# Optimization experiments

Measured on AMD Instinct MI355X. Metric: run time of the kernel, lower is better.

## Reference

```python
import jax, jax.numpy as jnp
import numpy as np

# DeepSeek-V2 MLA dims (one tensor-parallel shard of 8)
H = 5120          # hidden size
S = 2048          # seq len
B = 1
NH = 16           # 128 heads / 8 devices
Q_LORA = 1536
KV_LORA = 512
NOPE = 128
ROPE = 64
QK = NOPE + ROPE  # 192 per-head q/k dim
VD = 128          # v head dim
DEVICE_NUM = 8
EPS = 1e-6


def rms_norm(x, w):
    v = jnp.mean(jnp.square(x.astype(jnp.float32)), axis=-1, keepdims=True)
    return (x * jax.lax.rsqrt(v + EPS)).astype(x.dtype) * w


def rope_cos_sin(position_ids, dim=ROPE, base=10000.0):
    inv_freq = 1.0 / (base ** (jnp.arange(0, dim, 2, dtype=jnp.float32) / dim))
    freqs = position_ids.astype(jnp.float32)[..., None] * inv_freq       # [B,S,dim/2]
    emb = jnp.concatenate([freqs, freqs], axis=-1)                        # [B,S,dim]
    return jnp.cos(emb), jnp.sin(emb)


def apply_rope(x, cos, sin):
    # DeepSeek interleaved reorder: view(b,h,s,d//2,2).transpose(-1,-2).reshape
    b, h, s, d = x.shape
    x = x.reshape(b, h, s, d // 2, 2).transpose(0, 1, 2, 4, 3).reshape(b, h, s, d)
    x1, x2 = x[..., : d // 2], x[..., d // 2:]
    rot = jnp.concatenate([-x2, x1], axis=-1)
    return x * cos[:, None] + rot * sin[:, None]


def setup_inputs() -> dict:
    key = jax.random.key(0)
    ks = jax.random.split(key, 8)
    sc = 0.02
    hidden_states = jax.random.normal(ks[0], (B, S, H), dtype=jnp.float32)
    position_ids = jnp.arange(S, dtype=jnp.int64 if jax.config.jax_enable_x64 else jnp.int32)[None, :].repeat(B, 0)
    attention_mask = jnp.triu(jnp.full((S, S), -1e9, dtype=jnp.float32), 1)[None, None]
    return {
        "hidden_states": hidden_states,
        "position_ids": position_ids,
        "attention_mask": attention_mask,
        "ln_w": jnp.ones((H,), jnp.float32),
        "q_a_w": jax.random.normal(ks[1], (Q_LORA, H), jnp.float32) * sc,
        "q_a_ln_w": jnp.ones((Q_LORA,), jnp.float32),
        "q_b_w": jax.random.normal(ks[2], (NH * QK, Q_LORA), jnp.float32) * sc,
        "kv_a_w": jax.random.normal(ks[3], (KV_LORA + ROPE, H), jnp.float32) * sc,
        "kv_a_ln_w": jnp.ones((KV_LORA,), jnp.float32),
        "kv_b_w": jax.random.normal(ks[4], (NH * (NOPE + VD), KV_LORA), jnp.float32) * sc,
        "o_w": jax.random.normal(ks[5], (H, NH * VD), jnp.float32) * sc,
    }


def reference(hidden_states, position_ids, attention_mask, ln_w, q_a_w, q_a_ln_w,
              q_b_w, kv_a_w, kv_a_ln_w, kv_b_w, o_w):
    b, s, _ = hidden_states.shape
    residual = hidden_states * (1.0 / DEVICE_NUM)
    x = rms_norm(hidden_states, ln_w)

    # Q path: low-rank down-proj + RMSNorm + up-proj
    q = rms_norm(x @ q_a_w.T, q_a_ln_w) @ q_b_w.T                # [b,s,NH*QK]
    q = q.reshape(b, s, NH, QK).transpose(0, 2, 1, 3)            # [b,NH,s,QK]
    q_nope, q_pe = q[..., :NOPE], q[..., NOPE:]

    # KV path: compressed latent + shared rope key
    ckv = x @ kv_a_w.T                                           # [b,s,KV_LORA+ROPE]
    c_kv, k_pe = ckv[..., :KV_LORA], ckv[..., KV_LORA:]
    k_pe = k_pe.reshape(b, s, 1, ROPE).transpose(0, 2, 1, 3)     # [b,1,s,ROPE]
    kv = rms_norm(c_kv, kv_a_ln_w) @ kv_b_w.T                    # [b,s,NH*(NOPE+VD)]
    kv = kv.reshape(b, s, NH, NOPE + VD).transpose(0, 2, 1, 3)
    k_nope, v = kv[..., :NOPE], kv[..., NOPE:]

    cos, sin = rope_cos_sin(position_ids)
    q_pe = apply_rope(q_pe, cos, sin)
    k_pe = apply_rope(k_pe, cos, sin)

    k = jnp.concatenate([k_nope, jnp.broadcast_to(k_pe, (b, NH, s, ROPE))], axis=-1)
    qf = jnp.concatenate([q_nope, q_pe], axis=-1)

    scores = jnp.einsum('bhqd,bhkd->bhqk', qf, k) * (1.0 / np.sqrt(QK))
    scores = scores + attention_mask
    probs = jax.nn.softmax(scores, axis=-1)
    attn = jnp.einsum('bhqk,bhkd->bhqd', probs, v)               # [b,NH,s,VD]

    out = attn.transpose(0, 2, 1, 3).reshape(b, s, NH * VD) @ o_w.T
    hidden = residual + out
    return hidden.astype(jnp.float32), k.astype(jnp.float32), v.astype(jnp.float32)
```

## Files before the change

kernel.cpp:

```cpp
#include <hip/hip_runtime.h>
#include <math.h>

typedef unsigned short u16;
typedef unsigned int u32;
typedef __attribute__((ext_vector_type(8))) short short8;
typedef __attribute__((ext_vector_type(4))) float f32x4;

#define NHEADS 16
static const int S      = 2048;
static const int Hd     = 5120;
static const int QLORA  = 1536;
static const int KVLORA = 512;
static const int NQK    = 192;
static const int NVD    = 128;
static const int QDIM   = 3072;
static const int KVDIM  = 4096;
static const int NFUSE  = 2176;

__device__ __forceinline__ u16 f2bf(float f) {
    union { float f; u32 u; } v; v.f = f;
    u32 r = v.u + 0x7FFFu + ((v.u >> 16) & 1u);
    return (u16)(r >> 16);
}
__device__ __forceinline__ float bf2f(u16 h) {
    union { u32 u; float f; } v; v.u = (u32)h << 16; return v.f;
}

__global__ void convert_all_kernel(const float* __restrict__ o_w,
                                   const float* __restrict__ q_a_w,
                                   const float* __restrict__ kv_a_w,
                                   const float* __restrict__ q_b_w,
                                   const float* __restrict__ kv_b_w,
                                   u16* __restrict__ o_wb, u16* __restrict__ Wf,
                                   u16* __restrict__ q_b_wb, u16* __restrict__ kv_b_wb) {
    long c = (long)blockIdx.x * 256 + threadIdx.x;
    const float* src; u16* dst; long nsrcc;
    if (c < 2621440L)      { src = o_w;    dst = o_wb;            nsrcc = 2621440L; }
    else if (c < 4587520L) { c -= 2621440L; src = q_a_w; dst = Wf; nsrcc = 1966080L; }
    else if (c < 5406720L) { c -= 4587520L; src = kv_a_w; dst = Wf + 7864320L; nsrcc = 737280L; }
    else if (c < 6586368L) { c -= 5406720L; src = q_b_w;  dst = q_b_wb;  nsrcc = 1179648L; }
    else if (c < 7110656L) { c -= 6586368L; src = kv_b_w; dst = kv_b_wb; nsrcc = 524288L; }
    else return;
    union { u16 h[4]; uint2 u; } p;
    if (c < nsrcc) {
        float4 v = *(const float4*)(src + c * 4);
        p.h[0] = f2bf(v.x); p.h[1] = f2bf(v.y); p.h[2] = f2bf(v.z); p.h[3] = f2bf(v.w);
    } else {
        p.h[0] = p.h[1] = p.h[2] = p.h[3] = 0;
    }
    *(uint2*)(dst + c * 4) = p.u;
}

__global__ void rmsnorm_bf16_kernel(const float* in, const float* __restrict__ w,
                                    u16* out, int D, int in_stride, int out_stride) {
    int row = blockIdx.x;
    const float* x = in + (size_t)row * in_stride;
    u16* y = out + (size_t)row * out_stride;
    float ss = 0.f;
    for (int i = threadIdx.x; i < D; i += blockDim.x) { float v = x[i]; ss += v * v; }
    #pragma unroll
    for (int off = 32; off > 0; off >>= 1) ss += __shfl_xor(ss, off);
    __shared__ float wsum[8];
    int wid = threadIdx.x >> 6, lane = threadIdx.x & 63;
    if (lane == 0) wsum[wid] = ss;
    __syncthreads();
    float tot = 0.f;
    int nw = blockDim.x >> 6;
    for (int i = 0; i < nw; ++i) tot += wsum[i];
    float scale = rsqrtf(tot / (float)D + 1e-6f);
    for (int i = threadIdx.x; i < D; i += blockDim.x) y[i] = f2bf(x[i] * scale * w[i]);
}

__global__ void rms_qkv_kernel(const u16* __restrict__ CF,
                               const float* __restrict__ qw, const float* __restrict__ kw,
                               u16* __restrict__ QAn, u16* __restrict__ CKVN) {
    const int row = blockIdx.x;
    const u16* x; u16* y; const float* w; int D;
    if (blockIdx.y == 0) {
        x = CF + (size_t)row * NFUSE;          y = QAn + (size_t)row * QLORA;
        w = qw; D = QLORA;
    } else {
        x = CF + (size_t)row * NFUSE + QLORA;  y = CKVN + (size_t)row * KVLORA;
        w = kw; D = KVLORA;
    }
    float ss = 0.f;
    for (int i = threadIdx.x; i < D; i += blockDim.x) { float v = bf2f(x[i]); ss += v * v; }
    #pragma unroll
    for (int off = 32; off > 0; off >>= 1) ss += __shfl_xor(ss, off);
    __shared__ float wsum[4];
    int wid = threadIdx.x >> 6, lane = threadIdx.x & 63;
    if (lane == 0) wsum[wid] = ss;
    __syncthreads();
    float tot = wsum[0] + wsum[1] + wsum[2] + wsum[3];
    float scale = rsqrtf(tot / (float)D + 1e-6f);
    for (int i = threadIdx.x; i < D; i += blockDim.x) y[i] = f2bf(bf2f(x[i]) * scale * w[i]);
}

template<int BM, bool SWZ, bool OBF>
__global__ __launch_bounds__(256) void gemm64_k(
    const u16* __restrict__ A, const u16* __restrict__ B, void* __restrict__ Cv,
    int M, int N, int K, const float* __restrict__ resid) {
    constexpr int MR = BM / 32;
    constexpr int ALOADS = (BM * 128) / 4096;
    __shared__ u16 As[2][BM * 64];
    __shared__ u16 Bs[2][128 * 64];

    int bm, bn;
    if constexpr (SWZ) {
        const int lin = blockIdx.x + blockIdx.y * gridDim.x;
        const int nwg = gridDim.x * gridDim.y;
        const int xcd = lin & 7, off = lin >> 3;
        const int q = nwg >> 3, r = nwg & 7;
        const int wg = (xcd < r ? xcd * (q + 1) : r * (q + 1) + (xcd - r) * q) + off;
        bm = (wg % gridDim.y) * BM;
        bn = (wg / gridDim.y) * 128;
    } else {
        bm = blockIdx.y * BM;
        bn = blockIdx.x * 128;
    }

    const int tid = threadIdx.x;
    const int w = tid >> 6, lane = tid & 63;
    const int wr = w >> 1, wc = w & 1;
    const int fr = lane & 15, kg = lane >> 4;
    const int swz = (fr & 7) << 4;

    f32x4 acc[MR][4];
    #pragma unroll
    for (int i = 0; i < MR; ++i)
        #pragma unroll
        for (int j = 0; j < 4; ++j) acc[i][j] = (f32x4){0.f, 0.f, 0.f, 0.f};

    const size_t K2 = (size_t)K * 2;

    auto STAGE = [&](int buf, int kt) {
        const char* ga = (const char*)A + ((size_t)bm * K + (size_t)kt * 64) * 2;
        const char* gb = (const char*)B + ((size_t)bn * K + (size_t)kt * 64) * 2;
        #pragma unroll
        for (int j = 0; j < ALOADS; ++j) {
            const int D = j * 4096 + tid * 16;
            const int r = D >> 7, c = (D & 127) ^ ((r & 7) << 4);
            __builtin_amdgcn_global_load_lds(
                (const __attribute__((address_space(1))) void*)(ga + (size_t)r * K2 + c),
                (__attribute__((address_space(3))) void*)((char*)&As[buf][0] + D), 16, 0, 0);
        }
        #pragma unroll
        for (int j = 0; j < 4; ++j) {
            const int D = j * 4096 + tid * 16;
            const int r = D >> 7, c = (D & 127) ^ ((r & 7) << 4);
            __builtin_amdgcn_global_load_lds(
                (const __attribute__((address_space(1))) void*)(gb + (size_t)r * K2 + c),
                (__attribute__((address_space(3))) void*)((char*)&Bs[buf][0] + D), 16, 0, 0);
        }
    };
    auto COMP = [&](int buf) {
        #pragma unroll
        for (int s = 0; s < 2; ++s) {
            short8 af[MR], bfr[4];
            #pragma unroll
            for (int i = 0; i < MR; ++i) {
                const int row = wr * (BM / 2) + i * 16 + fr;
                af[i] = *(const short8*)((const char*)&As[buf][0] +
                         row * 128 + ((s * 64 + kg * 16) ^ swz));
            }
            #pragma unroll
            for (int i = 0; i < 4; ++i) {
                const int row = wc * 64 + i * 16 + fr;
                bfr[i] = *(const short8*)((const char*)&Bs[buf][0] +
                          row * 128 + ((s * 64 + kg * 16) ^ swz));
            }
            #pragma unroll
            for (int mi = 0; mi < MR; ++mi)
                #pragma unroll
                for (int ni = 0; ni < 4; ++ni)
                    acc[mi][ni] = __builtin_amdgcn_mfma_f32_16x16x32_bf16(
                        af[mi], bfr[ni], acc[mi][ni], 0, 0, 0);
        }
    };

    const int nk = K >> 6;
    STAGE(0, 0);
    asm volatile("s_waitcnt vmcnt(0)" ::: "memory");
    __builtin_amdgcn_s_barrier();
    for (int kt = 0; kt < nk; ++kt) {
        if (kt + 1 < nk) STAGE((kt + 1) & 1, kt + 1);
        COMP(kt & 1);
        asm volatile("s_waitcnt vmcnt(0)" ::: "memory");
        __builtin_amdgcn_s_barrier();
    }

    #pragma unroll
    for (int mi = 0; mi < MR; ++mi)
        #pragma unroll
        for (int ni = 0; ni < 4; ++ni)
            #pragma unroll
            for (int r2 = 0; r2 < 4; ++r2) {
                int row = bm + wr * (BM / 2) + mi * 16 + kg * 4 + r2;
                int col = bn + wc * 64 + ni * 16 + fr;
                size_t idx = (size_t)row * N + col;
                float v = acc[mi][ni][r2];
                if constexpr (OBF) {
                    ((u16*)Cv)[idx] = f2bf(v);
                } else {
                    if (resid) v += resid[idx] * 0.125f;
                    ((float*)Cv)[idx] = v;
                }
            }
}

__global__ __launch_bounds__(256) void gemm_qkv64_kernel(
    const u16* __restrict__ QAn, const u16* __restrict__ CKVN,
    const u16* __restrict__ q_b_wb, const u16* __restrict__ kv_b_wb,
    u16* __restrict__ Qbf, u16* __restrict__ KVb) {
    __shared__ u16 As[2][64 * 64];
    __shared__ u16 Bs[2][128 * 64];
    const bool isQ = blockIdx.x < 24;
    const u16* A = isQ ? QAn : CKVN;
    const u16* B = isQ ? q_b_wb : kv_b_wb;
    const int K = isQ ? QLORA : KVLORA;
    const int bn = (isQ ? blockIdx.x : blockIdx.x - 24) * 128;
    const int bm = blockIdx.y * 64;

    const int tid = threadIdx.x;
    const int w = tid >> 6, lane = tid & 63;
    const int wr = w >> 1, wc = w & 1;
    const int fr = lane & 15, kg = lane >> 4;
    const int swz = (fr & 7) << 4;

    f32x4 acc[2][4];
    #pragma unroll
    for (int i = 0; i < 2; ++i)
        #pragma unroll
        for (int j = 0; j < 4; ++j) acc[i][j] = (f32x4){0.f, 0.f, 0.f, 0.f};

    const size_t K2 = (size_t)K * 2;

    auto STAGE = [&](int buf, int kt) {
        const char* ga = (const char*)A + ((size_t)bm * K + (size_t)kt * 64) * 2;
        const char* gb = (const char*)B + ((size_t)bn * K + (size_t)kt * 64) * 2;
        #pragma unroll
        for (int j = 0; j < 2; ++j) {
            const int D = j * 4096 + tid * 16;
            const int r = D >> 7, c = (D & 127) ^ ((r & 7) << 4);
            __builtin_amdgcn_global_load_lds(
                (const __attribute__((address_space(1))) void*)(ga + (size_t)r * K2 + c),
                (__attribute__((address_space(3))) void*)((char*)&As[buf][0] + D), 16, 0, 0);
        }
        #pragma unroll
        for (int j = 0; j < 4; ++j) {
            const int D = j * 4096 + tid * 16;
            const int r = D >> 7, c = (D & 127) ^ ((r & 7) << 4);
            __builtin_amdgcn_global_load_lds(
                (const __attribute__((address_space(1))) void*)(gb + (size_t)r * K2 + c),
                (__attribute__((address_space(3))) void*)((char*)&Bs[buf][0] + D), 16, 0, 0);
        }
    };
    auto COMP = [&](int buf) {
        #pragma unroll
        for (int s = 0; s < 2; ++s) {
            short8 af[2], bfr[4];
            #pragma unroll
            for (int i = 0; i < 2; ++i) {
                const int row = wr * 32 + i * 16 + fr;
                af[i] = *(const short8*)((const char*)&As[buf][0] +
                         row * 128 + ((s * 64 + kg * 16) ^ swz));
            }
            #pragma unroll
            for (int i = 0; i < 4; ++i) {
                const int row = wc * 64 + i * 16 + fr;
                bfr[i] = *(const short8*)((const char*)&Bs[buf][0] +
                          row * 128 + ((s * 64 + kg * 16) ^ swz));
            }
            #pragma unroll
            for (int mi = 0; mi < 2; ++mi)
                #pragma unroll
                for (int ni = 0; ni < 4; ++ni)
                    acc[mi][ni] = __builtin_amdgcn_mfma_f32_16x16x32_bf16(
                        af[mi], bfr[ni], acc[mi][ni], 0, 0, 0);
        }
    };

    const int nk = K >> 6;
    STAGE(0, 0);
    asm volatile("s_waitcnt vmcnt(0)" ::: "memory");
    __builtin_amdgcn_s_barrier();
    for (int kt = 0; kt < nk; ++kt) {
        if (kt + 1 < nk) STAGE((kt + 1) & 1, kt + 1);
        COMP(kt & 1);
        asm volatile("s_waitcnt vmcnt(0)" ::: "memory");
        __builtin_amdgcn_s_barrier();
    }

    #pragma unroll
    for (int mi = 0; mi < 2; ++mi)
        #pragma unroll
        for (int ni = 0; ni < 4; ++ni)
            #pragma unroll
            for (int r2 = 0; r2 < 4; ++r2) {
                int row = bm + wr * 32 + mi * 16 + kg * 4 + r2;
                int col = bn + wc * 64 + ni * 16 + fr;
                float v = acc[mi][ni][r2];
                if (isQ) {
                    size_t idx = ((size_t)(col / 192) * S + row) * 192 + (col % 192);
                    Qbf[idx] = f2bf(v);
                } else {
                    KVb[(size_t)row * KVDIM + col] = f2bf(v);
                }
            }
}

__global__ void rope_q_inplace_kernel(u16* __restrict__ Qbf, const int* __restrict__ pos) {
    const int s = blockIdx.x;
    const int t = threadIdx.x;
    const int hh = t >> 5, j = t & 31;
    float ps = (float)pos[s];
    float inv_freq = 1.0f / powf(10000.0f, (float)j * (1.0f / 32.0f));
    float ang = ps * inv_freq;
    float c = cosf(ang), sn = sinf(ang);
    u16* base = Qbf + ((size_t)hh * S + s) * NQK;
    float a = bf2f(base[128 + 2 * j]), b = bf2f(base[128 + 2 * j + 1]);
    __syncthreads();
    base[128 + j] = f2bf(a * c - b * sn);
    base[160 + j] = f2bf(b * c + a * sn);
}

__global__ __launch_bounds__(256) void build_kv64_kernel(
    const u16* __restrict__ KVb, const u16* __restrict__ CF,
    const int* __restrict__ pos_ids,
    float* __restrict__ Kout, float* __restrict__ Vout,
    u16* __restrict__ Kbf, u16* __restrict__ Vtb) {
    const int s0 = blockIdx.x * 64;
    const int h  = blockIdx.y;
    const int t  = threadIdx.x;
    __shared__ u16 T[64][132];

    #pragma unroll
    for (int it = 0; it < 4; ++it) {
        int i = t + it * 256;
        int row = i >> 4, c8 = (i & 15) * 8;
        int s = s0 + row;
        union { uint4 u; u16 hx[8]; } v;
        v.u = *(const uint4*)(KVb + (size_t)s * KVDIM + h * 256 + c8);
        size_t kidx = ((size_t)h * S + s) * NQK + c8;
        *(uint4*)(Kbf + kidx) = v.u;
        float4 f0 = {bf2f(v.hx[0]), bf2f(v.hx[1]), bf2f(v.hx[2]), bf2f(v.hx[3])};
        float4 f1 = {bf2f(v.hx[4]), bf2f(v.hx[5]), bf2f(v.hx[6]), bf2f(v.hx[7])};
        *(float4*)(Kout + kidx) = f0;
        *(float4*)(Kout + kidx + 4) = f1;
    }
    #pragma unroll
    for (int it = 0; it < 4; ++it) {
        int i = t + it * 256;
        int row = i >> 4, c8 = (i & 15) * 8;
        int s = s0 + row;
        union { uint4 u; uint2 d[2]; u16 hx[8]; } v;
        v.u = *(const uint4*)(KVb + (size_t)s * KVDIM + h * 256 + 128 + c8);
        *(uint2*)&T[row][c8]     = v.d[0];
        *(uint2*)&T[row][c8 + 4] = v.d[1];
        size_t vidx = ((size_t)h * S + s) * NVD + c8;
        float4 f0 = {bf2f(v.hx[0]), bf2f(v.hx[1]), bf2f(v.hx[2]), bf2f(v.hx[3])};
        float4 f1 = {bf2f(v.hx[4]), bf2f(v.hx[5]), bf2f(v.hx[6]), bf2f(v.hx[7])};
        *(float4*)(Vout + vidx) = f0;
        *(float4*)(Vout + vidx + 4) = f1;
    }
    #pragma unroll
    for (int it = 0; it < 8; ++it) {
        int i = t + it * 256;
        int row = i >> 5, j = i & 31;
        int s = s0 + row;
        float ps = (float)pos_ids[s];
        float inv_freq = 1.0f / powf(10000.0f, (float)j * (1.0f / 32.0f));
        float ang = ps * inv_freq;
        float c = cosf(ang), sn = sinf(ang);
        u32 pr = *(const u32*)(CF + (size_t)s * NFUSE + QLORA + KVLORA + 2 * j);
        float a = bf2f((u16)pr), b = bf2f((u16)(pr >> 16));
        float k0 = a * c - b * sn;
        float k1 = b * c + a * sn;
        size_t kidx = ((size_t)h * S + s) * NQK;
        Kout[kidx + 128 + j] = k0;
        Kout[kidx + 160 + j] = k1;
        Kbf[kidx + 128 + j] = f2bf(k0);
        Kbf[kidx + 160 + j] = f2bf(k1);
    }
    __syncthreads();
    const int d = t >> 1, half = t & 1;
    #pragma unroll
    for (int c = 0; c < 4; ++c) {
        u16 tmp[8];
        #pragma unroll
        for (int e = 0; e < 8; ++e) tmp[e] = T[half * 32 + c * 8 + e][d];
        *(uint4*)(Vtb + ((size_t)h * NVD + d) * S + s0 + half * 32 + c * 8) = *(uint4*)tmp;
    }
}

__global__ __launch_bounds__(256) void attn_mfma_kernel(
    const u16* __restrict__ Qbf, const u16* __restrict__ Kb,
    const u16* __restrict__ Vtb, u16* __restrict__ ATb) {
    const int h = blockIdx.y;
    const int q0 = (gridDim.x - 1 - blockIdx.x) * 64;
    const int tid = threadIdx.x;
    const int w = tid >> 6, lane = tid & 63;
    const int fr = lane & 15, kg = lane >> 4;

    __shared__ __align__(16) u16 Ks[2][64 * 192];
    __shared__ __align__(16) u16 Vts[2][128 * 64];

    int kSrc[6], vSrc[4];
    #pragma unroll
    for (int i = 0; i < 6; ++i) {
        int D = (w * 6 + i) * 1024 + lane * 16;
        int row = D / 384, wb = D - row * 384;
        kSrc[i] = row * 384 + (wb ^ ((row & 7) << 4));
    }
    #pragma unroll
    for (int i = 0; i < 4; ++i) {
        int D = (w * 4 + i) * 1024 + lane * 16;
        int row = D >> 7, wb = D & 127;
        vSrc[i] = row * (S * 2) + (wb ^ ((row & 7) << 4));
    }
    const char* Kg = (const char*)(Kb + (size_t)h * S * NQK);
    const char* Vg = (const char*)(Vtb + (size_t)h * NVD * S);

    auto STAGE = [&](int buf, int kt) {
        const size_t krow = (size_t)kt * 64;
        #pragma unroll
        for (int i = 0; i < 6; ++i)
            __builtin_amdgcn_global_load_lds(
                (const __attribute__((address_space(1))) void*)(Kg + krow * 384 + kSrc[i]),
                (__attribute__((address_space(3))) void*)((char*)&Ks[buf][0] + (w * 6 + i) * 1024), 16, 0, 0);
        #pragma unroll
        for (int i = 0; i < 4; ++i)
            __builtin_amdgcn_global_load_lds(
                (const __attribute__((address_space(1))) void*)(Vg + krow * 2 + vSrc[i]),
                (__attribute__((address_space(3))) void*)((char*)&Vts[buf][0] + (w * 4 + i) * 1024), 16, 0, 0);
    };

    short8 qf[6];
    {
        const u16* qrow = Qbf + ((size_t)h * S + q0 + w * 16 + fr) * NQK;
        #pragma unroll
        for (int kb = 0; kb < 6; ++kb)
            qf[kb] = *(const short8*)(qrow + kb * 32 + kg * 8);
    }

    f32x4 o[8];
    #pragma unroll
    for (int ni = 0; ni < 8; ++ni) o[ni] = (f32x4){0.f, 0.f, 0.f, 0.f};
    float mrow = -1e30f, lrow = 0.f;
    const float scale = 0.0721687836487032f;
    const int qg = q0 + w * 16 + fr;
    const int swz = (fr & 7) << 4;
    const int nt = (q0 >> 6) + 1;

    STAGE(0, 0);
    asm volatile("s_waitcnt vmcnt(0)" ::: "memory");
    __builtin_amdgcn_s_barrier();

    for (int t = 0; t < nt; ++t) {
        if (t + 1 < nt) STAGE((t + 1) & 1, t + 1);
        const int buf = t & 1;
        const int k0 = t * 64;

        f32x4 sacc[4];
        #pragma unroll
        for (int mi = 0; mi < 4; ++mi) sacc[mi] = (f32x4){0.f, 0.f, 0.f, 0.f};
        __builtin_amdgcn_s_setprio(1);
        #pragma unroll
        for (int mi = 0; mi < 4; ++mi)
            #pragma unroll
            for (int kb = 0; kb < 6; ++kb) {
                const short8 kf = *(const short8*)((const char*)&Ks[buf][0] +
                    (mi * 16 + fr) * 384 + ((kb * 64 + kg * 16) ^ swz));
                sacc[mi] = __builtin_amdgcn_mfma_f32_16x16x32_bf16(kf, qf[kb], sacc[mi], 0, 0, 0);
            }
        __builtin_amdgcn_s_setprio(0);

        const bool diag = (k0 == q0);
        float p[4][4];
        float mx = -1e30f;
        #pragma unroll
        for (int mi = 0; mi < 4; ++mi)
            #pragma unroll
            for (int r = 0; r < 4; ++r) {
                float v = sacc[mi][r] * scale;
                if (diag && (k0 + mi * 16 + kg * 4 + r > qg)) v = -1e30f;
                p[mi][r] = v;
                mx = fmaxf(mx, v);
            }
        mx = fmaxf(mx, __shfl_xor(mx, 16));
        mx = fmaxf(mx, __shfl_xor(mx, 32));
        const bool noresc = __all(mx <= mrow + 8.0f);
        float mnew = noresc ? mrow : fmaxf(mrow, mx);
        float psum = 0.f;
        #pragma unroll
        for (int mi = 0; mi < 4; ++mi)
            #pragma unroll
            for (int r = 0; r < 4; ++r) {
                float e = __expf(p[mi][r] - mnew);
                p[mi][r] = e;
                psum += e;
            }
        psum += __shfl_xor(psum, 16);
        psum += __shfl_xor(psum, 32);
        if (noresc) {
            lrow += psum;
        } else {
            float corr = __expf(mrow - mnew);
            lrow = lrow * corr + psum;
            mrow = mnew;
            float corr_r[4];
            #pragma unroll
            for (int r = 0; r < 4; ++r) corr_r[r] = __shfl(corr, kg * 4 + r);
            #pragma unroll
            for (int ni = 0; ni < 8; ++ni) {
                o[ni][0] *= corr_r[0]; o[ni][1] *= corr_r[1];
                o[ni][2] *= corr_r[2]; o[ni][3] *= corr_r[3];
            }
        }

        u32 pk0[4], pk1[4];
        #pragma unroll
        for (int mi = 0; mi < 4; ++mi) {
            pk0[mi] = (u32)f2bf(p[mi][0]) | ((u32)f2bf(p[mi][1]) << 16);
            pk1[mi] = (u32)f2bf(p[mi][2]) | ((u32)f2bf(p[mi][3]) << 16);
        }
        const int srcA = 2 * (kg & 1) * 16 + fr;
        const int srcB = srcA + 16;
        const int hsel = kg >> 1;
        short8 pa[2];
        #pragma unroll
        for (int ks = 0; ks < 2; ++ks) {
            u32 a0 = (u32)__shfl((int)pk0[ks * 2], srcA), b0 = (u32)__shfl((int)pk0[ks * 2 + 1], srcA);
            u32 a1 = (u32)__shfl((int)pk1[ks * 2], srcA), b1 = (u32)__shfl((int)pk1[ks * 2 + 1], srcA);
            u32 a2 = (u32)__shfl((int)pk0[ks * 2], srcB), b2 = (u32)__shfl((int)pk0[ks * 2 + 1], srcB);
            u32 a3 = (u32)__shfl((int)pk1[ks * 2], srcB), b3 = (u32)__shfl((int)pk1[ks * 2 + 1], srcB);
            union { u32 u[4]; short8 s8; } cvt;
            cvt.u[0] = hsel ? b0 : a0;
            cvt.u[1] = hsel ? b1 : a1;
            cvt.u[2] = hsel ? b2 : a2;
            cvt.u[3] = hsel ? b3 : a3;
            pa[ks] = cvt.s8;
        }

        __builtin_amdgcn_s_setprio(1);
        #pragma unroll
        for (int ks = 0; ks < 2; ++ks)
            #pragma unroll
            for (int ni = 0; ni < 8; ++ni) {
                const short8 vf = *(const short8*)((const char*)&Vts[buf][0] +
                    (ni * 16 + fr) * 128 + ((ks * 64 + kg * 16) ^ swz));
                o[ni] = __builtin_amdgcn_mfma_f32_16x16x32_bf16(pa[ks], vf, o[ni], 0, 0, 0);
            }
        __builtin_amdgcn_s_setprio(0);

        asm volatile("s_waitcnt vmcnt(0)" ::: "memory");
        __builtin_amdgcn_s_barrier();
    }

    float inv = 1.f / lrow;
    float inv_r[4];
    #pragma unroll
    for (int r = 0; r < 4; ++r) inv_r[r] = __shfl(inv, kg * 4 + r);
    u16* outp = ATb + (size_t)(q0 + w * 16 + kg * 4) * (NHEADS * NVD) + h * NVD + fr;
    #pragma unroll
    for (int ni = 0; ni < 8; ++ni)
        #pragma unroll
        for (int r = 0; r < 4; ++r)
            outp[(size_t)r * (NHEADS * NVD) + ni * 16] = f2bf(o[ni][r] * inv_r[r]);
}

extern "C" void kernel_launch(void* const* d_in, const int* in_sizes, int n_in,
                              void* d_out, int out_size, void* d_ws, size_t ws_size,
                              hipStream_t stream) {
    (void)in_sizes; (void)n_in; (void)out_size; (void)ws_size;
    const float* hidden    = (const float*)d_in[0];
    const int*   pos       = (const int*)d_in[1];
    const float* ln_w      = (const float*)d_in[3];
    const float* q_a_w     = (const float*)d_in[4];
    const float* q_a_ln_w  = (const float*)d_in[5];
    const float* q_b_w     = (const float*)d_in[6];
    const float* kv_a_w    = (const float*)d_in[7];
    const float* kv_a_ln_w = (const float*)d_in[8];
    const float* kv_b_w    = (const float*)d_in[9];
    const float* o_w       = (const float*)d_in[10];

    float* OUT_H = (float*)d_out;
    float* OUT_K = OUT_H + (size_t)S * Hd;
    float* OUT_V = OUT_K + (size_t)NHEADS * S * NQK;

    char* ws = (char*)d_ws;
    u16*   o_wb    = (u16*)(ws);
    u16*   Wf      = (u16*)(ws + 20971520);
    u16*   Qbf     = (u16*)(ws + 20971520);
    u16*   Vtb     = (u16*)(ws + 33554432);
    u16*   Xb      = (u16*)(ws + 43253760);
    u16*   Kbf     = (u16*)(ws + 43253760);
    u16*   ATb     = (u16*)(ws + 55836672);
    u16*   CF      = (u16*)(ws + 64225280);
    u16*   QAn     = (u16*)(ws + 73138176);
    u16*   CKVN    = (u16*)(ws + 79429632);
    u16*   q_b_wb  = (u16*)(ws + 81526784);
    u16*   kv_b_wb = (u16*)(ws + 90963968);
    u16*   KVb     = (u16*)(ws + 95158272);

    convert_all_kernel<<<27776, 256, 0, stream>>>(o_w, q_a_w, kv_a_w, q_b_w, kv_b_w,
                                                  o_wb, Wf, q_b_wb, kv_b_wb);
    rmsnorm_bf16_kernel<<<S, 256, 0, stream>>>(hidden, ln_w, Xb, Hd, Hd, Hd);
    gemm64_k<128, true, true><<<dim3(NFUSE / 128, S / 128), 256, 0, stream>>>(Xb, Wf, CF, S, NFUSE, Hd, nullptr);
    rms_qkv_kernel<<<dim3(S, 2), 256, 0, stream>>>(CF, q_a_ln_w, kv_a_ln_w, QAn, CKVN);
    gemm_qkv64_kernel<<<dim3(56, S / 64), 256, 0, stream>>>(QAn, CKVN, q_b_wb, kv_b_wb, Qbf, KVb);
    rope_q_inplace_kernel<<<S, 512, 0, stream>>>(Qbf, pos);
    build_kv64_kernel<<<dim3(S / 64, NHEADS), 256, 0, stream>>>(KVb, CF, pos, OUT_K, OUT_V, Kbf, Vtb);
    attn_mfma_kernel<<<dim3(S / 64, NHEADS), 256, 0, stream>>>(Qbf, Kbf, Vtb, ATb);
    gemm64_k<64, false, false><<<dim3(Hd / 128, S / 64), 256, 0, stream>>>(ATb, o_wb, OUT_H, S, Hd, NHEADS * NVD, hidden);
}
```

Baseline: 376.7 us.

## Split causal attention over KV chunks with separate combine kernel

Splits each query tile's causal KV range into chunks of up to eight tiles, so long query tiles are processed by several blocks and work per head is balanced across 80 blocks. Partial outputs, row maxima and sums are written in fp32 to workspace and merged by a new combine kernel that normalises and writes bf16. The lazy-rescale shortcut is also replaced by unconditional rescaling. This adds fp32 partial-result traffic and an extra launch in exchange for better load balance and occupancy.

```diff
diff --git a/kernel.cpp b/kernel.cpp
--- a/kernel.cpp
+++ b/kernel.cpp
@@ -393,11 +393,21 @@
     }
 }
 
-__global__ __launch_bounds__(256) void attn_mfma_kernel(
+__global__ __launch_bounds__(256) void attn_split_kernel(
     const u16* __restrict__ Qbf, const u16* __restrict__ Kb,
-    const u16* __restrict__ Vtb, u16* __restrict__ ATb) {
+    const u16* __restrict__ Vtb, float* __restrict__ PO,
+    float* __restrict__ PM, float* __restrict__ PL) {
     const int h = blockIdx.y;
-    const int q0 = (gridDim.x - 1 - blockIdx.x) * 64;
+    const int bx = blockIdx.x;
+    int qt, ch;
+    if (bx < 8)       { qt = bx;                 ch = 0; }
+    else if (bx < 24) { qt = 8 + ((bx - 8) >> 1);  ch = (bx - 8) & 1; }
+    else if (bx < 48) { qt = 16 + (bx - 24) / 3;   ch = (bx - 24) % 3; }
+    else              { qt = 24 + ((bx - 48) >> 2); ch = (bx - 48) & 3; }
+    const int q0 = qt * 64;
+    const int tStart = ch * 8;
+    const int cnt = min(tStart + 8, qt + 1) - tStart;
+
     const int tid = threadIdx.x;
     const int w = tid >> 6, lane = tid & 63;
     const int fr = lane & 15, kg = lane >> 4;
@@ -450,15 +460,15 @@
     const float scale = 0.0721687836487032f;
     const int qg = q0 + w * 16 + fr;
     const int swz = (fr & 7) << 4;
-    const int nt = (q0 >> 6) + 1;
-
-    STAGE(0, 0);
+
+    STAGE(0, tStart);
     asm volatile("s_waitcnt vmcnt(0)" ::: "memory");
     __builtin_amdgcn_s_barrier();
 
-    for (int t = 0; t < nt; ++t) {
-        if (t + 1 < nt) STAGE((t + 1) & 1, t + 1);
-        const int buf = t & 1;
+    for (int it = 0; it < cnt; ++it) {
+        const int t = tStart + it;
+        if (it + 1 < cnt) STAGE((it + 1) & 1, t + 1);
+        const int buf = it & 1;
         const int k0 = t * 64;
 
         f32x4 sacc[4];
@@ -489,8 +499,8 @@
             }
         mx = fmaxf(mx, __shfl_xor(mx, 16));
         mx = fmaxf(mx, __shfl_xor(mx, 32));
-        const bool noresc = __all(mx <= mrow + 8.0f);
-        float mnew = noresc ? mrow : fmaxf(mrow, mx);
+        float mnew = fmaxf(mrow, mx);
+        float corr = __expf(mrow - mnew);
         float psum = 0.f;
         #pragma unroll
         for (int mi = 0; mi < 4; ++mi)
@@ -502,20 +512,15 @@
             }
         psum += __shfl_xor(psum, 16);
         psum += __shfl_xor(psum, 32);
-        if (noresc) {
-            lrow += psum;
-        } else {
-            float corr = __expf(mrow - mnew);
-            lrow = lrow * corr + psum;
-            mrow = mnew;
-            float corr_r[4];
-            #pragma unroll
-            for (int r = 0; r < 4; ++r) corr_r[r] = __shfl(corr, kg * 4 + r);
-            #pragma unroll
-            for (int ni = 0; ni < 8; ++ni) {
-                o[ni][0] *= corr_r[0]; o[ni][1] *= corr_r[1];
-                o[ni][2] *= corr_r[2]; o[ni][3] *= corr_r[3];
-            }
+        lrow = lrow * corr + psum;
+        mrow = mnew;
+        float corr_r[4];
+        #pragma unroll
+        for (int r = 0; r < 4; ++r) corr_r[r] = __shfl(corr, kg * 4 + r);
+        #pragma unroll
+        for (int ni = 0; ni < 8; ++ni) {
+            o[ni][0] *= corr_r[0]; o[ni][1] *= corr_r[1];
+            o[ni][2] *= corr_r[2]; o[ni][3] *= corr_r[3];
         }
 
         u32 pk0[4], pk1[4];
@@ -557,16 +562,61 @@
         __builtin_amdgcn_s_barrier();
     }
 
-    float inv = 1.f / lrow;
-    float inv_r[4];
-    #pragma unroll
-    for (int r = 0; r < 4; ++r) inv_r[r] = __shfl(inv, kg * 4 + r);
-    u16* outp = ATb + (size_t)(q0 + w * 16 + kg * 4) * (NHEADS * NVD) + h * NVD + fr;
+    const int slot = h * 80 + bx;
+    float* po = PO + (size_t)slot * (64 * 128);
     #pragma unroll
     for (int ni = 0; ni < 8; ++ni)
         #pragma unroll
         for (int r = 0; r < 4; ++r)
-            outp[(size_t)r * (NHEADS * NVD) + ni * 16] = f2bf(o[ni][r] * inv_r[r]);
+            po[(size_t)(w * 16 + kg * 4 + r) * 128 + ni * 16 + fr] = o[ni][r];
+    if (kg == 0) {
+        PM[slot * 64 + w * 16 + fr] = mrow;
+        PL[slot * 64 + w * 16 + fr] = lrow;
+    }
+}
+
+__global__ __launch_bounds__(256) void attn_combine_kernel(
+    const float* __restrict__ PO, const float* __restrict__ PM,
+    const float* __restrict__ PL, u16* __restrict__ ATb) {
+    const int qt = blockIdx.x, h = blockIdx.y;
+    const int nch = (qt >> 3) + 1;
+    const int off = qt < 8 ? qt : qt < 16 ? 8 + 2 * (qt - 8)
+                  : qt < 24 ? 24 + 3 * (qt - 16) : 48 + 4 * (qt - 24);
+    const int slot0 = h * 80 + off;
+    const int t = threadIdx.x;
+    const int r = t >> 2, cg = (t & 3) * 32;
+
+    float m0 = PM[(size_t)slot0 * 64 + r], l0 = PL[(size_t)slot0 * 64 + r];
+    float m1 = -1e30f, l1 = 0.f, m2 = -1e30f, l2 = 0.f, m3 = -1e30f, l3 = 0.f;
+    if (nch > 1) { m1 = PM[(size_t)(slot0 + 1) * 64 + r]; l1 = PL[(size_t)(slot0 + 1) * 64 + r]; }
+    if (nch > 2) { m2 = PM[(size_t)(slot0 + 2) * 64 + r]; l2 = PL[(size_t)(slot0 + 2) * 64 + r]; }
+    if (nch > 3) { m3 = PM[(size_t)(slot0 + 3) * 64 + r]; l3 = PL[(size_t)(slot0 + 3) * 64 + r]; }
+    float M = fmaxf(fmaxf(m0, m1), fmaxf(m2, m3));
+    float s0 = __expf(m0 - M), s1 = __expf(m1 - M), s2 = __expf(m2 - M), s3 = __expf(m3 - M);
+    float L = l0 * s0 + l1 * s1 + l2 * s2 + l3 * s3;
+    float invL = 1.f / L;
+
+    const float* p0 = PO + ((size_t)slot0 * 64 + r) * 128 + cg;
+    u16* outp = ATb + (size_t)(qt * 64 + r) * (NHEADS * NVD) + h * NVD + cg;
+    #pragma unroll
+    for (int j = 0; j < 32; j += 4) {
+        float4 v = *(const float4*)(p0 + j);
+        float4 a = {v.x * s0, v.y * s0, v.z * s0, v.w * s0};
+        if (nch > 1) {
+            float4 u = *(const float4*)(p0 + 64 * 128 + j);
+            a.x += u.x * s1; a.y += u.y * s1; a.z += u.z * s1; a.w += u.w * s1;
+        }
+        if (nch > 2) {
+            float4 u = *(const float4*)(p0 + 2 * 64 * 128 + j);
+            a.x += u.x * s2; a.y += u.y * s2; a.z += u.z * s2; a.w += u.w * s2;
+        }
+        if (nch > 3) {
+            float4 u = *(const float4*)(p0 + 3 * 64 * 128 + j);
+            a.x += u.x * s3; a.y += u.y * s3; a.z += u.z * s3; a.w += u.w * s3;
+        }
+        u16 pk[4] = {f2bf(a.x * invL), f2bf(a.y * invL), f2bf(a.z * invL), f2bf(a.w * invL)};
+        *(uint2*)(outp + j) = *(uint2*)pk;
+    }
 }
 
 extern "C" void kernel_launch(void* const* d_in, const int* in_sizes, int n_in,
@@ -602,6 +652,9 @@
     u16*   q_b_wb  = (u16*)(ws + 81526784);
     u16*   kv_b_wb = (u16*)(ws + 90963968);
     u16*   KVb     = (u16*)(ws + 95158272);
+    float* PO      = (float*)(ws + 64225280);
+    float* PM      = (float*)(ws + 106168320);
+    float* PL      = (float*)(ws + 106496000);
 
     convert_all_kernel<<<27776, 256, 0, stream>>>(o_w, q_a_w, kv_a_w, q_b_w, kv_b_w,
                                                   o_wb, Wf, q_b_wb, kv_b_wb);
@@ -611,6 +664,7 @@
     gemm_qkv64_kernel<<<dim3(56, S / 64), 256, 0, stream>>>(QAn, CKVN, q_b_wb, kv_b_wb, Qbf, KVb);
     rope_q_inplace_kernel<<<S, 512, 0, stream>>>(Qbf, pos);
     build_kv64_kernel<<<dim3(S / 64, NHEADS), 256, 0, stream>>>(KVb, CF, pos, OUT_K, OUT_V, Kbf, Vtb);
-    attn_mfma_kernel<<<dim3(S / 64, NHEADS), 256, 0, stream>>>(Qbf, Kbf, Vtb, ATb);
+    attn_split_kernel<<<dim3(80, NHEADS), 256, 0, stream>>>(Qbf, Kbf, Vtb, PO, PM, PL);
+    attn_combine_kernel<<<dim3(32, NHEADS), 256, 0, stream>>>(PO, PM, PL, ATb);
     gemm64_k<64, false, false><<<dim3(Hd / 128, S / 64), 256, 0, stream>>>(ATb, o_wb, OUT_H, S, Hd, NHEADS * NVD, hidden);
 }
```

New measurement: 391.5 us. +3.9%, slower.
